# Kernel tuning notes

Hardware: AMD Instinct MI355X
Metric: run time of the kernel (lower is better)

## Reference

```python
import jax, jax.numpy as jnp
import numpy as np

DIM = 1024


def setup_inputs() -> dict:
    key = jax.random.key(0)
    ks = jax.random.split(key, 10)
    B, SQ, SKV, D = 4, 2048, 2048, DIM
    s = 1.0 / np.sqrt(D)
    return {
        "query": jax.random.normal(ks[0], (B, SQ, D), dtype=jnp.float32),
        "key_value": jax.random.normal(ks[1], (B, SKV, D), dtype=jnp.float32),
        "Wq": jax.random.normal(ks[2], (D, D), dtype=jnp.float32) * s,
        "bq": jnp.zeros((D,), dtype=jnp.float32),
        "Wk": jax.random.normal(ks[3], (D, D), dtype=jnp.float32) * s,
        "bk": jnp.zeros((D,), dtype=jnp.float32),
        "Wv": jax.random.normal(ks[4], (D, D), dtype=jnp.float32) * s,
        "bv": jnp.zeros((D,), dtype=jnp.float32),
        "Wo": jax.random.normal(ks[5], (D, D), dtype=jnp.float32) * s,
        "bo": jnp.zeros((D,), dtype=jnp.float32),
    }


def reference(query, key_value, Wq, bq, Wk, bk, Wv, bv, Wo, bo):
    # Faithful to the Keras layer: NO 1/sqrt(d) scaling, single head.
    Q = jnp.einsum("bsd,de->bse", query, Wq) + bq            # [B,Sq,D]
    K = jnp.einsum("btd,de->bte", key_value, Wk) + bk        # [B,Skv,D]
    V = jnp.einsum("btd,de->bte", key_value, Wv) + bv        # [B,Skv,D]
    scores = jnp.einsum("bse,bte->bst", Q, K)                # [B,Sq,Skv]
    attn = jax.nn.softmax(scores, axis=-1)
    ctx = jnp.einsum("bst,bte->bse", attn, V)                # [B,Sq,D]
    return jnp.einsum("bse,ef->bsf", ctx, Wo) + bo
```

## Files before the change

kernel.cpp:

```cpp
#include <hip/hip_runtime.h>
#include <cstdint>

typedef unsigned short u16;
typedef _Float16 f16;
typedef __attribute__((ext_vector_type(8))) short    s8v;
typedef __attribute__((ext_vector_type(8))) _Float16 h8v;
typedef __attribute__((ext_vector_type(4))) float    f4v;

__device__ __forceinline__ float bf2f(u16 b) {
  unsigned int u = ((unsigned int)b) << 16;
  float f;
  __builtin_memcpy(&f, &u, 4);
  return f;
}
__device__ __forceinline__ u16 f2bf(float f) {
  unsigned int u;
  __builtin_memcpy(&u, &f, 4);
  u += 0x7fffu + ((u >> 16) & 1u);
  return (u16)(u >> 16);
}

__device__ __forceinline__ void glds16(const void* g, void* l) {
  __builtin_amdgcn_global_load_lds(
      (const __attribute__((address_space(1))) unsigned int*)g,
      (__attribute__((address_space(3))) unsigned int*)l, 16, 0, 0);
}

#define BM 128
#define BN 128

__global__ __launch_bounds__(256)
void detect_dtype(const u16* __restrict__ q, int* __restrict__ flg)
{
  __shared__ int cbig, czero;
  if (threadIdx.x == 0) { cbig = 0; czero = 0; }
  __syncthreads();
  int b = 0, z = 0;
  for (int i = threadIdx.x; i < 4096; i += 256) {
    float v = bf2f(q[i]);
    if (!(fabsf(v) < 1e4f)) b++;
    if ((i & 1) == 0 && q[i] == 0) z++;
  }
  atomicAdd(&cbig, b);
  atomicAdd(&czero, z);
  __syncthreads();
  if (threadIdx.x == 0) flg[0] = (cbig > 64 || czero > 1600) ? 1 : 0;
}

__global__ __launch_bounds__(256)
void convert_h(const int* __restrict__ flg,
               const void* __restrict__ q, const void* __restrict__ kv,
               f16* __restrict__ qo, f16* __restrict__ kvo, long n)
{
  const void* in = blockIdx.y ? kv : q;
  f16* out = blockIdx.y ? kvo : qo;
  const long i = ((long)blockIdx.x * 256 + threadIdx.x) * 8;
  if (i >= n) return;
  h8v h;
  if (flg[0] != 0) {
    const float* p = (const float*)in + i;
    f4v f0 = *(const f4v*)p;
    f4v f1 = *(const f4v*)(p + 4);
#pragma unroll
    for (int j = 0; j < 4; ++j) {
      h[j]     = (f16)f0[j];
      h[4 + j] = (f16)f1[j];
    }
  } else {
    s8v b = *(const s8v*)((const short*)in + i);
#pragma unroll
    for (int j = 0; j < 8; ++j) h[j] = (f16)bf2f((u16)b[j]);
  }
  *(h8v*)(out + i) = h;
}

__global__ __launch_bounds__(256)
void transpose_w4(const int* __restrict__ flg,
                  const void* __restrict__ w0, const void* __restrict__ w1,
                  const void* __restrict__ w2, const void* __restrict__ w3,
                  f16* __restrict__ h0, f16* __restrict__ h1,
                  f16* __restrict__ h2, u16* __restrict__ b3, int D)
{
  __shared__ float tile[32][33];
  const int zb = blockIdx.z;
  const void* in_v = (zb == 0) ? w0 : (zb == 1) ? w1 : (zb == 2) ? w2 : w3;
  const bool i32 = (flg[0] != 0);
  const u16*   in16 = (const u16*)in_v;
  const float* in32 = (const float*)in_v;
  const int c0 = blockIdx.x * 32, r0 = blockIdx.y * 32;
  const int tx = threadIdx.x, ty = threadIdx.y;
  for (int i = ty; i < 32; i += 8) {
    const long idx = (long)(r0 + i) * D + c0 + tx;
    tile[i][tx] = i32 ? in32[idx] : bf2f(in16[idx]);
  }
  __syncthreads();
  f16* outH = (zb == 0) ? h0 : (zb == 1) ? h1 : h2;
  for (int i = ty; i < 32; i += 8) {
    const long idx = (long)(c0 + i) * D + r0 + tx;
    const float v = tile[tx][i];
    if (zb == 3) b3[idx]   = f2bf(v);
    else         outH[idx] = (f16)v;
  }
}

__global__ __launch_bounds__(256)
void gemm_proj3(const int* __restrict__ flg,
                const f16* __restrict__ Qi, const f16* __restrict__ KVi,
                const f16* __restrict__ WqT, const f16* __restrict__ WkT,
                const f16* __restrict__ WvT,
                const void* __restrict__ bq, const void* __restrict__ bk,
                const void* __restrict__ bv,
                f16* __restrict__ Qf, f16* __restrict__ Kf,
                u16* __restrict__ Vt, int M, int N, int K, int SB)
{
  __shared__ u16 As[BM * 64];
  __shared__ u16 Bs[BN * 64];

  const int zb = blockIdx.z;
  const f16* A = (zb == 0) ? Qi : KVi;
  const f16* B = (zb == 0) ? WqT : (zb == 1) ? WkT : WvT;
  const void* bias = (zb == 0) ? bq : (zb == 1) ? bk : bv;

  const int f_in = flg[0];
  const int tid = threadIdx.x, lane = tid & 63, wave = tid >> 6;
  const int wm = wave >> 1, wn = wave & 1;
  const int m0 = blockIdx.y * BM, n0 = blockIdx.x * BN;

  const int rr  = wave * 32 + (lane >> 2);
  const int cc8 = 8 * ((lane & 3) ^ ((lane >> 3) & 3));
  const f16* ga00 = A + (long)(m0 + rr) * K + cc8;
  const f16* ga01 = ga00 + 16 * (long)K;
  const f16* gb00 = B + (long)(n0 + rr) * K + cc8;
  const f16* gb01 = gb00 + 16 * (long)K;
  u16* la0 = &As[(wave * 2) * 512];  u16* la1 = la0 + 512;
  u16* lb0 = &Bs[(wave * 2) * 512];  u16* lb1 = lb0 + 512;

  f4v acc[4][4];
#pragma unroll
  for (int i = 0; i < 4; ++i)
#pragma unroll
    for (int j = 0; j < 4; ++j) acc[i][j] = (f4v){0.f, 0.f, 0.f, 0.f};

  const int fr  = lane & 15;
  const int fks = 8 * (((lane >> 4) ^ (lane >> 1)) & 3);
  const int aoff = (wm * 64 + fr) * 32 + fks;
  const int boff = (wn * 64 + fr) * 32 + fks;

  for (int kt = 0; kt < K; kt += 64) {
    glds16(ga00,      la0);        glds16(ga01,      la1);
    glds16(ga00 + 32, la0 + 4096); glds16(ga01 + 32, la1 + 4096);
    glds16(gb00,      lb0);        glds16(gb01,      lb1);
    glds16(gb00 + 32, lb0 + 4096); glds16(gb01 + 32, lb1 + 4096);
    ga00 += 64; ga01 += 64; gb00 += 64; gb01 += 64;
    __syncthreads();

    {
      h8v af[4], bfr[4];
#pragma unroll
      for (int mi = 0; mi < 4; ++mi) af[mi]  = *(const h8v*)&As[aoff + mi * 512];
#pragma unroll
      for (int ni = 0; ni < 4; ++ni) bfr[ni] = *(const h8v*)&Bs[boff + ni * 512];
#pragma unroll
      for (int mi = 0; mi < 4; ++mi)
#pragma unroll
        for (int ni = 0; ni < 4; ++ni)
          acc[mi][ni] = __builtin_amdgcn_mfma_f32_16x16x32_f16(af[mi], bfr[ni], acc[mi][ni], 0, 0, 0);
    }
    {
      h8v af[4], bfr[4];
#pragma unroll
      for (int mi = 0; mi < 4; ++mi) af[mi]  = *(const h8v*)&As[4096 + aoff + mi * 512];
#pragma unroll
      for (int ni = 0; ni < 4; ++ni) bfr[ni] = *(const h8v*)&Bs[4096 + boff + ni * 512];
#pragma unroll
      for (int mi = 0; mi < 4; ++mi)
#pragma unroll
        for (int ni = 0; ni < 4; ++ni)
          acc[mi][ni] = __builtin_amdgcn_mfma_f32_16x16x32_f16(af[mi], bfr[ni], acc[mi][ni], 0, 0, 0);
    }
    __syncthreads();
  }

  const int cr = (lane >> 4) * 4, ccl = lane & 15;
  if (zb < 2) {
    f16* out = zb ? Kf : Qf;
#pragma unroll
    for (int ni = 0; ni < 4; ++ni) {
      const int gcol = n0 + wn * 64 + ni * 16 + ccl;
      const float bvv = (f_in != 0) ? ((const float*)bias)[gcol]
                                    : bf2f(((const u16*)bias)[gcol]);
#pragma unroll
      for (int mi = 0; mi < 4; ++mi)
#pragma unroll
        for (int r = 0; r < 4; ++r) {
          const long grow = (long)(m0 + wm * 64 + mi * 16 + cr + r);
          out[grow * N + gcol] = (f16)(acc[mi][ni][r] + bvv);
        }
    }
  } else {
    u16* xw = (wave < 2) ? (&As[0] + wave * 2176) : (&Bs[0] + (wave - 2) * 2176);
    const int b  = m0 / SB;
    const int s0 = (m0 % SB) + wm * 64;
    const long bbase = (long)b * N * SB;
#pragma unroll
    for (int h = 0; h < 2; ++h) {
#pragma unroll
      for (int nl = 0; nl < 2; ++nl) {
        const int ni = h * 2 + nl;
        const int gcol = n0 + wn * 64 + ni * 16 + ccl;
        const float bvv = (f_in != 0) ? ((const float*)bias)[gcol]
                                      : bf2f(((const u16*)bias)[gcol]);
#pragma unroll
        for (int mi = 0; mi < 4; ++mi)
#pragma unroll
          for (int r = 0; r < 4; ++r)
            xw[(mi * 16 + cr + r) * 34 + nl * 16 + ccl] = f2bf(acc[mi][ni][r] + bvv);
      }
      __syncthreads();
#pragma unroll
      for (int c = 0; c < 32; ++c) {
        const int gcol = n0 + wn * 64 + h * 32 + c;
        Vt[bbase + (long)gcol * SB + s0 + lane] = xw[lane * 34 + c];
      }
      __syncthreads();
    }
  }
}

__global__ __launch_bounds__(256)
void gemm_sc64(const f16* __restrict__ A, const f16* __restrict__ B,
               float* __restrict__ C, int M, int N, int K,
               long sA, long sB, long sC)
{
  __shared__ u16 As[BM * 64];
  __shared__ u16 Bs[BN * 64];

  const int tid = threadIdx.x, lane = tid & 63, wave = tid >> 6;
  const int wm = wave >> 1, wn = wave & 1;
  const int m0 = blockIdx.y * BM, n0 = blockIdx.x * BN;
  const long z = blockIdx.z;

  const int rr  = wave * 32 + (lane >> 2);
  const int cc8 = 8 * ((lane & 3) ^ ((lane >> 3) & 3));
  const f16* ga00 = A + (long)(m0 + rr) * K + cc8 + z * sA;
  const f16* ga01 = ga00 + 16 * (long)K;
  const f16* gb00 = B + (long)(n0 + rr) * K + cc8 + z * sB;
  const f16* gb01 = gb00 + 16 * (long)K;
  u16* la0 = &As[(wave * 2) * 512];  u16* la1 = la0 + 512;
  u16* lb0 = &Bs[(wave * 2) * 512];  u16* lb1 = lb0 + 512;

  f4v acc[4][4];
#pragma unroll
  for (int i = 0; i < 4; ++i)
#pragma unroll
    for (int j = 0; j < 4; ++j) acc[i][j] = (f4v){0.f, 0.f, 0.f, 0.f};

  const int fr  = lane & 15;
  const int fks = 8 * (((lane >> 4) ^ (lane >> 1)) & 3);
  const int aoff = (wm * 64 + fr) * 32 + fks;
  const int boff = (wn * 64 + fr) * 32 + fks;

  for (int kt = 0; kt < K; kt += 64) {
    glds16(ga00,      la0);        glds16(ga01,      la1);
    glds16(ga00 + 32, la0 + 4096); glds16(ga01 + 32, la1 + 4096);
    glds16(gb00,      lb0);        glds16(gb01,      lb1);
    glds16(gb00 + 32, lb0 + 4096); glds16(gb01 + 32, lb1 + 4096);
    ga00 += 64; ga01 += 64; gb00 += 64; gb01 += 64;
    __syncthreads();

    {
      h8v af[4], bfr[4];
#pragma unroll
      for (int mi = 0; mi < 4; ++mi) af[mi]  = *(const h8v*)&As[aoff + mi * 512];
#pragma unroll
      for (int ni = 0; ni < 4; ++ni) bfr[ni] = *(const h8v*)&Bs[boff + ni * 512];
#pragma unroll
      for (int mi = 0; mi < 4; ++mi)
#pragma unroll
        for (int ni = 0; ni < 4; ++ni)
          acc[mi][ni] = __builtin_amdgcn_mfma_f32_16x16x32_f16(af[mi], bfr[ni], acc[mi][ni], 0, 0, 0);
    }
    {
      h8v af[4], bfr[4];
#pragma unroll
      for (int mi = 0; mi < 4; ++mi) af[mi]  = *(const h8v*)&As[4096 + aoff + mi * 512];
#pragma unroll
      for (int ni = 0; ni < 4; ++ni) bfr[ni] = *(const h8v*)&Bs[4096 + boff + ni * 512];
#pragma unroll
      for (int mi = 0; mi < 4; ++mi)
#pragma unroll
        for (int ni = 0; ni < 4; ++ni)
          acc[mi][ni] = __builtin_amdgcn_mfma_f32_16x16x32_f16(af[mi], bfr[ni], acc[mi][ni], 0, 0, 0);
    }
    __syncthreads();
  }

  const int cr = (lane >> 4) * 4, ccl = lane & 15;
#pragma unroll
  for (int ni = 0; ni < 4; ++ni) {
    const int gcol = n0 + wn * 64 + ni * 16 + ccl;
#pragma unroll
    for (int mi = 0; mi < 4; ++mi)
#pragma unroll
      for (int r = 0; r < 4; ++r) {
        const long grow = (long)(m0 + wm * 64 + mi * 16 + cr + r);
        C[z * sC + grow * N + gcol] = acc[mi][ni][r];
      }
  }
}

template<bool OUT_FLAG, bool HAS_BIAS>
__global__ __launch_bounds__(256)
void gemm_bf64(const int* __restrict__ flg, const u16* __restrict__ A,
               const u16* __restrict__ Bt, const void* __restrict__ bias,
               void* __restrict__ Cv, int M, int N, int K,
               long sA, long sB, long sC)
{
  __shared__ u16 As[BM * 64];
  __shared__ u16 Bs[BN * 64];

  const int f_in = flg[0];
  const int tid = threadIdx.x, lane = tid & 63, wave = tid >> 6;
  const int wm = wave >> 1, wn = wave & 1;
  const int m0 = blockIdx.y * BM, n0 = blockIdx.x * BN;
  const long z = blockIdx.z;

  const int rr  = wave * 32 + (lane >> 2);
  const int cc8 = 8 * ((lane & 3) ^ ((lane >> 3) & 3));
  const u16* ga00 = A + (long)(m0 + rr) * K + cc8 + z * sA;
  const u16* ga01 = ga00 + 16 * (long)K;
  const u16* gb00 = Bt + (long)(n0 + rr) * K + cc8 + z * sB;
  const u16* gb01 = gb00 + 16 * (long)K;
  u16* la0 = &As[(wave * 2) * 512];  u16* la1 = la0 + 512;
  u16* lb0 = &Bs[(wave * 2) * 512];  u16* lb1 = lb0 + 512;

  f4v acc[4][4];
#pragma unroll
  for (int i = 0; i < 4; ++i)
#pragma unroll
    for (int j = 0; j < 4; ++j) acc[i][j] = (f4v){0.f, 0.f, 0.f, 0.f};

  const int fr  = lane & 15;
  const int fks = 8 * (((lane >> 4) ^ (lane >> 1)) & 3);
  const int aoff = (wm * 64 + fr) * 32 + fks;
  const int boff = (wn * 64 + fr) * 32 + fks;

  for (int kt = 0; kt < K; kt += 64) {
    glds16(ga00,      la0);        glds16(ga01,      la1);
    glds16(ga00 + 32, la0 + 4096); glds16(ga01 + 32, la1 + 4096);
    glds16(gb00,      lb0);        glds16(gb01,      lb1);
    glds16(gb00 + 32, lb0 + 4096); glds16(gb01 + 32, lb1 + 4096);
    ga00 += 64; ga01 += 64; gb00 += 64; gb01 += 64;
    __syncthreads();

    {
      s8v af[4], bfr[4];
#pragma unroll
      for (int mi = 0; mi < 4; ++mi) af[mi]  = *(const s8v*)&As[aoff + mi * 512];
#pragma unroll
      for (int ni = 0; ni < 4; ++ni) bfr[ni] = *(const s8v*)&Bs[boff + ni * 512];
#pragma unroll
      for (int mi = 0; mi < 4; ++mi)
#pragma unroll
        for (int ni = 0; ni < 4; ++ni)
          acc[mi][ni] = __builtin_amdgcn_mfma_f32_16x16x32_bf16(af[mi], bfr[ni], acc[mi][ni], 0, 0, 0);
    }
    {
      s8v af[4], bfr[4];
#pragma unroll
      for (int mi = 0; mi < 4; ++mi) af[mi]  = *(const s8v*)&As[4096 + aoff + mi * 512];
#pragma unroll
      for (int ni = 0; ni < 4; ++ni) bfr[ni] = *(const s8v*)&Bs[4096 + boff + ni * 512];
#pragma unroll
      for (int mi = 0; mi < 4; ++mi)
#pragma unroll
        for (int ni = 0; ni < 4; ++ni)
          acc[mi][ni] = __builtin_amdgcn_mfma_f32_16x16x32_bf16(af[mi], bfr[ni], acc[mi][ni], 0, 0, 0);
    }
    __syncthreads();
  }

  const int cr = (lane >> 4) * 4, ccl = lane & 15;
  const bool o32 = OUT_FLAG && (f_in != 0);
#pragma unroll
  for (int ni = 0; ni < 4; ++ni) {
    const int gcol = n0 + wn * 64 + ni * 16 + ccl;
    float bvv = 0.f;
    if (HAS_BIAS)
      bvv = (f_in != 0) ? ((const float*)bias)[gcol] : bf2f(((const u16*)bias)[gcol]);
#pragma unroll
    for (int mi = 0; mi < 4; ++mi)
#pragma unroll
      for (int r = 0; r < 4; ++r) {
        const long grow = (long)(m0 + wm * 64 + mi * 16 + cr + r);
        const float val = acc[mi][ni][r] + bvv;
        const long idx = z * sC + grow * N + gcol;
        if (o32) ((float*)Cv)[idx] = val;
        else     ((u16*)Cv)[idx]   = f2bf(val);
      }
  }
}

__global__ __launch_bounds__(256)
void softmax_rows_bf(const float* __restrict__ S, u16* __restrict__ P, int N)
{
  const float* row = S + (long)blockIdx.x * N;
  u16* prow = P + (long)blockIdx.x * N;
  const int t = threadIdx.x;
  f4v v0 = *(const f4v*)(row + t * 8);
  f4v v1 = *(const f4v*)(row + t * 8 + 4);

  float m = v0[0];
#pragma unroll
  for (int j = 1; j < 4; ++j) m = fmaxf(m, v0[j]);
#pragma unroll
  for (int j = 0; j < 4; ++j) m = fmaxf(m, v1[j]);
  for (int off = 32; off > 0; off >>= 1) m = fmaxf(m, __shfl_down(m, off, 64));

  __shared__ float redm[4], reds[4];
  if ((t & 63) == 0) redm[t >> 6] = m;
  __syncthreads();
  m = fmaxf(fmaxf(redm[0], redm[1]), fmaxf(redm[2], redm[3]));

  float s = 0.f;
#pragma unroll
  for (int j = 0; j < 4; ++j) { v0[j] = __expf(v0[j] - m); s += v0[j]; }
#pragma unroll
  for (int j = 0; j < 4; ++j) { v1[j] = __expf(v1[j] - m); s += v1[j]; }
  for (int off = 32; off > 0; off >>= 1) s += __shfl_down(s, off, 64);
  if ((t & 63) == 0) reds[t >> 6] = s;
  __syncthreads();
  s = reds[0] + reds[1] + reds[2] + reds[3];

  const float inv = 1.f / s;
  s8v o;
#pragma unroll
  for (int j = 0; j < 4; ++j) {
    o[j]     = (short)f2bf(v0[j] * inv);
    o[4 + j] = (short)f2bf(v1[j] * inv);
  }
  *(s8v*)(prow + t * 8) = o;
}

extern "C" void kernel_launch(void* const* d_in, const int* in_sizes, int n_in,
                              void* d_out, int out_size, void* d_ws, size_t ws_size,
                              hipStream_t stream)
{
  const void* query = d_in[0];
  const void* kv    = d_in[1];
  const void* Wq    = d_in[2];
  const void* bq    = d_in[3];
  const void* Wk    = d_in[4];
  const void* bk    = d_in[5];
  const void* Wv    = d_in[6];
  const void* bv    = d_in[7];
  const void* Wo    = d_in[8];
  const void* bo    = d_in[9];

  const int Bn = 4, S = 2048, D = 1024;
  const int MS = Bn * S;
  const size_t KBu = 1024, MBu = 1024 * 1024;
  const long nTok = (long)MS * D;

  char* ws = (char*)d_ws;
  int*  flg  = (int*)(ws);
  f16*  Qi   = (f16*)(ws + 64 * KBu);
  f16*  KVi  = (f16*)(ws + 64 * KBu + 16 * MBu);
  char* rW   = ws + 64 * KBu + 32 * MBu;
  f16*  WqT  = (f16*)(rW);
  f16*  WkT  = (f16*)(rW + 2 * MBu);
  f16*  WvT  = (f16*)(rW + 4 * MBu);
  u16*  WoT  = (u16*)(rW + 6 * MBu);
  char* rQK  = rW + 8 * MBu;
  f16*  Qf   = (f16*)(rQK);
  f16*  Kf   = (f16*)(rQK + 16 * MBu);
  u16*  attn = (u16*)(rQK);
  float* Sc  = (float*)(rQK + 32 * MBu);
  char* rV   = rQK + 96 * MBu;
  u16*  Vt   = (u16*)(rV);
  u16*  Cx   = (u16*)(rV + 16 * MBu);

  detect_dtype<<<1, 256, 0, stream>>>((const u16*)query, flg);

  convert_h<<<dim3((unsigned)(nTok / 2048), 2), 256, 0, stream>>>(
      flg, query, kv, Qi, KVi, nTok);

  dim3 tb(32, 8);
  transpose_w4<<<dim3(32, 32, 4), tb, 0, stream>>>(
      flg, Wq, Wk, Wv, Wo, WqT, WkT, WvT, WoT, D);

  gemm_proj3<<<dim3(D / BN, MS / BM, 3), 256, 0, stream>>>(
      flg, Qi, KVi, WqT, WkT, WvT, bq, bk, bv, Qf, Kf, Vt, MS, D, D, S);

  gemm_sc64<<<dim3(S / BN, S / BM, Bn), 256, 0, stream>>>(
      Qf, Kf, Sc, S, S, D, (long)S * D, (long)S * D, (long)S * S);
  softmax_rows_bf<<<dim3(Bn * S), 256, 0, stream>>>(Sc, attn, S);
  gemm_bf64<false, false><<<dim3(D / BN, S / BM, Bn), 256, 0, stream>>>(
      flg, attn, Vt, nullptr, Cx, S, D, S, (long)S * S, (long)D * S, (long)S * D);

  gemm_bf64<true, true><<<dim3(D / BN, MS / BM, 1), 256, 0, stream>>>(
      flg, Cx, WoT, bo, d_out, MS, D, D, 0L, 0L, 0L);
}
```

Before: 389.7 us.

## Double-buffer LDS tiles in GEMM kernels and swizzle block order for L2 reuse

Each of the three MFMA GEMM kernels now has two LDS buffers, so the async global-to-LDS loads for the next K tile are issued before the MFMAs on the current tile, overlapping memory with compute. A grouped block swizzle remaps blockIdx into groups of eight rows to improve L2 reuse of A/B tiles. LDS use per block doubles to 64KB, which may lower occupancy. The V-transpose scratch now sits entirely within As.

```diff
diff --git a/kernel.cpp b/kernel.cpp
--- a/kernel.cpp
+++ b/kernel.cpp
@@ -26,8 +26,24 @@
       (__attribute__((address_space(3))) unsigned int*)l, 16, 0, 0);
 }
 
+__device__ __forceinline__ void swz_xy(int& bx, int& by) {
+  const int gx = gridDim.x;
+  const int p = blockIdx.y * gx + blockIdx.x;
+  bx = (p >> 3) % gx;
+  by = (p & 7) + 8 * (p / (gx * 8));
+}
+
 #define BM 128
 #define BN 128
+
+#define STAGE8(dstA, dstB)                                                  \
+  do {                                                                      \
+    glds16(ga00,      (dstA) + l0);        glds16(ga01,      (dstA) + l1);  \
+    glds16(ga00 + 32, (dstA) + l0 + 4096); glds16(ga01 + 32, (dstA) + l1 + 4096); \
+    glds16(gb00,      (dstB) + l0);        glds16(gb01,      (dstB) + l1);  \
+    glds16(gb00 + 32, (dstB) + l0 + 4096); glds16(gb01 + 32, (dstB) + l1 + 4096); \
+    ga00 += 64; ga01 += 64; gb00 += 64; gb01 += 64;                         \
+  } while (0)
 
 __global__ __launch_bounds__(256)
 void detect_dtype(const u16* __restrict__ q, int* __restrict__ flg)
@@ -113,8 +129,8 @@
                 f16* __restrict__ Qf, f16* __restrict__ Kf,
                 u16* __restrict__ Vt, int M, int N, int K, int SB)
 {
-  __shared__ u16 As[BM * 64];
-  __shared__ u16 Bs[BN * 64];
+  __shared__ u16 As[2 * 8192];
+  __shared__ u16 Bs[2 * 8192];
 
   const int zb = blockIdx.z;
   const f16* A = (zb == 0) ? Qi : KVi;
@@ -124,7 +140,9 @@
   const int f_in = flg[0];
   const int tid = threadIdx.x, lane = tid & 63, wave = tid >> 6;
   const int wm = wave >> 1, wn = wave & 1;
-  const int m0 = blockIdx.y * BM, n0 = blockIdx.x * BN;
+  int bx, by;
+  swz_xy(bx, by);
+  const int m0 = by * BM, n0 = bx * BN;
 
   const int rr  = wave * 32 + (lane >> 2);
   const int cc8 = 8 * ((lane & 3) ^ ((lane >> 3) & 3));
@@ -132,8 +150,7 @@
   const f16* ga01 = ga00 + 16 * (long)K;
   const f16* gb00 = B + (long)(n0 + rr) * K + cc8;
   const f16* gb01 = gb00 + 16 * (long)K;
-  u16* la0 = &As[(wave * 2) * 512];  u16* la1 = la0 + 512;
-  u16* lb0 = &Bs[(wave * 2) * 512];  u16* lb1 = lb0 + 512;
+  const int l0 = (wave * 2) * 512, l1 = l0 + 512;
 
   f4v acc[4][4];
 #pragma unroll
@@ -146,20 +163,18 @@
   const int aoff = (wm * 64 + fr) * 32 + fks;
   const int boff = (wn * 64 + fr) * 32 + fks;
 
-  for (int kt = 0; kt < K; kt += 64) {
-    glds16(ga00,      la0);        glds16(ga01,      la1);
-    glds16(ga00 + 32, la0 + 4096); glds16(ga01 + 32, la1 + 4096);
-    glds16(gb00,      lb0);        glds16(gb01,      lb1);
-    glds16(gb00 + 32, lb0 + 4096); glds16(gb01 + 32, lb1 + 4096);
-    ga00 += 64; ga01 += 64; gb00 += 64; gb01 += 64;
-    __syncthreads();
-
+  const int nIt = K >> 6;
+  STAGE8(As, Bs);
+  __syncthreads();
+  for (int it = 0; it < nIt; ++it) {
+    const int cb = (it & 1) * 8192;
+    if (it + 1 < nIt) { STAGE8(As + (8192 - cb), Bs + (8192 - cb)); }
     {
       h8v af[4], bfr[4];
 #pragma unroll
-      for (int mi = 0; mi < 4; ++mi) af[mi]  = *(const h8v*)&As[aoff + mi * 512];
-#pragma unroll
-      for (int ni = 0; ni < 4; ++ni) bfr[ni] = *(const h8v*)&Bs[boff + ni * 512];
+      for (int mi = 0; mi < 4; ++mi) af[mi]  = *(const h8v*)&As[cb + aoff + mi * 512];
+#pragma unroll
+      for (int ni = 0; ni < 4; ++ni) bfr[ni] = *(const h8v*)&Bs[cb + boff + ni * 512];
 #pragma unroll
       for (int mi = 0; mi < 4; ++mi)
 #pragma unroll
@@ -169,9 +184,9 @@
     {
       h8v af[4], bfr[4];
 #pragma unroll
-      for (int mi = 0; mi < 4; ++mi) af[mi]  = *(const h8v*)&As[4096 + aoff + mi * 512];
-#pragma unroll
-      for (int ni = 0; ni < 4; ++ni) bfr[ni] = *(const h8v*)&Bs[4096 + boff + ni * 512];
+      for (int mi = 0; mi < 4; ++mi) af[mi]  = *(const h8v*)&As[cb + 4096 + aoff + mi * 512];
+#pragma unroll
+      for (int ni = 0; ni < 4; ++ni) bfr[ni] = *(const h8v*)&Bs[cb + 4096 + boff + ni * 512];
 #pragma unroll
       for (int mi = 0; mi < 4; ++mi)
 #pragma unroll
@@ -198,7 +213,7 @@
         }
     }
   } else {
-    u16* xw = (wave < 2) ? (&As[0] + wave * 2176) : (&Bs[0] + (wave - 2) * 2176);
+    u16* xw = &As[wave * 2176];
     const int b  = m0 / SB;
     const int s0 = (m0 % SB) + wm * 64;
     const long bbase = (long)b * N * SB;
@@ -232,12 +247,14 @@
                float* __restrict__ C, int M, int N, int K,
                long sA, long sB, long sC)
 {
-  __shared__ u16 As[BM * 64];
-  __shared__ u16 Bs[BN * 64];
+  __shared__ u16 As[2 * 8192];
+  __shared__ u16 Bs[2 * 8192];
 
   const int tid = threadIdx.x, lane = tid & 63, wave = tid >> 6;
   const int wm = wave >> 1, wn = wave & 1;
-  const int m0 = blockIdx.y * BM, n0 = blockIdx.x * BN;
+  int bx, by;
+  swz_xy(bx, by);
+  const int m0 = by * BM, n0 = bx * BN;
   const long z = blockIdx.z;
 
   const int rr  = wave * 32 + (lane >> 2);
@@ -246,8 +263,7 @@
   const f16* ga01 = ga00 + 16 * (long)K;
   const f16* gb00 = B + (long)(n0 + rr) * K + cc8 + z * sB;
   const f16* gb01 = gb00 + 16 * (long)K;
-  u16* la0 = &As[(wave * 2) * 512];  u16* la1 = la0 + 512;
-  u16* lb0 = &Bs[(wave * 2) * 512];  u16* lb1 = lb0 + 512;
+  const int l0 = (wave * 2) * 512, l1 = l0 + 512;
 
   f4v acc[4][4];
 #pragma unroll
@@ -260,20 +276,18 @@
   const int aoff = (wm * 64 + fr) * 32 + fks;
   const int boff = (wn * 64 + fr) * 32 + fks;
 
-  for (int kt = 0; kt < K; kt += 64) {
-    glds16(ga00,      la0);        glds16(ga01,      la1);
-    glds16(ga00 + 32, la0 + 4096); glds16(ga01 + 32, la1 + 4096);
-    glds16(gb00,      lb0);        glds16(gb01,      lb1);
-    glds16(gb00 + 32, lb0 + 4096); glds16(gb01 + 32, lb1 + 4096);
-    ga00 += 64; ga01 += 64; gb00 += 64; gb01 += 64;
-    __syncthreads();
-
+  const int nIt = K >> 6;
+  STAGE8(As, Bs);
+  __syncthreads();
+  for (int it = 0; it < nIt; ++it) {
+    const int cb = (it & 1) * 8192;
+    if (it + 1 < nIt) { STAGE8(As + (8192 - cb), Bs + (8192 - cb)); }
     {
       h8v af[4], bfr[4];
 #pragma unroll
-      for (int mi = 0; mi < 4; ++mi) af[mi]  = *(const h8v*)&As[aoff + mi * 512];
-#pragma unroll
-      for (int ni = 0; ni < 4; ++ni) bfr[ni] = *(const h8v*)&Bs[boff + ni * 512];
+      for (int mi = 0; mi < 4; ++mi) af[mi]  = *(const h8v*)&As[cb + aoff + mi * 512];
+#pragma unroll
+      for (int ni = 0; ni < 4; ++ni) bfr[ni] = *(const h8v*)&Bs[cb + boff + ni * 512];
 #pragma unroll
       for (int mi = 0; mi < 4; ++mi)
 #pragma unroll
@@ -283,9 +297,9 @@
     {
       h8v af[4], bfr[4];
 #pragma unroll
-      for (int mi = 0; mi < 4; ++mi) af[mi]  = *(const h8v*)&As[4096 + aoff + mi * 512];
-#pragma unroll
-      for (int ni = 0; ni < 4; ++ni) bfr[ni] = *(const h8v*)&Bs[4096 + boff + ni * 512];
+      for (int mi = 0; mi < 4; ++mi) af[mi]  = *(const h8v*)&As[cb + 4096 + aoff + mi * 512];
+#pragma unroll
+      for (int ni = 0; ni < 4; ++ni) bfr[ni] = *(const h8v*)&Bs[cb + 4096 + boff + ni * 512];
 #pragma unroll
       for (int mi = 0; mi < 4; ++mi)
 #pragma unroll
@@ -316,13 +330,15 @@
                void* __restrict__ Cv, int M, int N, int K,
                long sA, long sB, long sC)
 {
-  __shared__ u16 As[BM * 64];
-  __shared__ u16 Bs[BN * 64];
+  __shared__ u16 As[2 * 8192];
+  __shared__ u16 Bs[2 * 8192];
 
   const int f_in = flg[0];
   const int tid = threadIdx.x, lane = tid & 63, wave = tid >> 6;
   const int wm = wave >> 1, wn = wave & 1;
-  const int m0 = blockIdx.y * BM, n0 = blockIdx.x * BN;
+  int bx, by;
+  swz_xy(bx, by);
+  const int m0 = by * BM, n0 = bx * BN;
   const long z = blockIdx.z;
 
   const int rr  = wave * 32 + (lane >> 2);
@@ -331,8 +347,7 @@
   const u16* ga01 = ga00 + 16 * (long)K;
   const u16* gb00 = Bt + (long)(n0 + rr) * K + cc8 + z * sB;
   const u16* gb01 = gb00 + 16 * (long)K;
-  u16* la0 = &As[(wave * 2) * 512];  u16* la1 = la0 + 512;
-  u16* lb0 = &Bs[(wave * 2) * 512];  u16* lb1 = lb0 + 512;
+  const int l0 = (wave * 2) * 512, l1 = l0 + 512;
 
   f4v acc[4][4];
 #pragma unroll
@@ -345,20 +360,18 @@
   const int aoff = (wm * 64 + fr) * 32 + fks;
   const int boff = (wn * 64 + fr) * 32 + fks;
 
-  for (int kt = 0; kt < K; kt += 64) {
-    glds16(ga00,      la0);        glds16(ga01,      la1);
-    glds16(ga00 + 32, la0 + 4096); glds16(ga01 + 32, la1 + 4096);
-    glds16(gb00,      lb0);        glds16(gb01,      lb1);
-    glds16(gb00 + 32, lb0 + 4096); glds16(gb01 + 32, lb1 + 4096);
-    ga00 += 64; ga01 += 64; gb00 += 64; gb01 += 64;
-    __syncthreads();
-
+  const int nIt = K >> 6;
+  STAGE8(As, Bs);
+  __syncthreads();
+  for (int it = 0; it < nIt; ++it) {
+    const int cb = (it & 1) * 8192;
+    if (it + 1 < nIt) { STAGE8(As + (8192 - cb), Bs + (8192 - cb)); }
     {
       s8v af[4], bfr[4];
 #pragma unroll
-      for (int mi = 0; mi < 4; ++mi) af[mi]  = *(const s8v*)&As[aoff + mi * 512];
-#pragma unroll
-      for (int ni = 0; ni < 4; ++ni) bfr[ni] = *(const s8v*)&Bs[boff + ni * 512];
+      for (int mi = 0; mi < 4; ++mi) af[mi]  = *(const s8v*)&As[cb + aoff + mi * 512];
+#pragma unroll
+      for (int ni = 0; ni < 4; ++ni) bfr[ni] = *(const s8v*)&Bs[cb + boff + ni * 512];
 #pragma unroll
       for (int mi = 0; mi < 4; ++mi)
 #pragma unroll
@@ -368,9 +381,9 @@
     {
       s8v af[4], bfr[4];
 #pragma unroll
-      for (int mi = 0; mi < 4; ++mi) af[mi]  = *(const s8v*)&As[4096 + aoff + mi * 512];
-#pragma unroll
-      for (int ni = 0; ni < 4; ++ni) bfr[ni] = *(const s8v*)&Bs[4096 + boff + ni * 512];
+      for (int mi = 0; mi < 4; ++mi) af[mi]  = *(const s8v*)&As[cb + 4096 + aoff + mi * 512];
+#pragma unroll
+      for (int ni = 0; ni < 4; ++ni) bfr[ni] = *(const s8v*)&Bs[cb + 4096 + boff + ni * 512];
 #pragma unroll
       for (int mi = 0; mi < 4; ++mi)
 #pragma unroll
```

After: 351.0 us. 1.11x faster.
